# Kernel optimization log

Hardware: AMD Instinct MI355X
Metric: run time of the kernel (lower is better)

## Reference

```python
import jax, jax.numpy as jnp
import numpy as np

N_GROUPS = 32
EPS = 1e-5


def group_norm(x, gamma, beta):
    b, c, h, w = x.shape
    xg = x.reshape(b, N_GROUPS, c // N_GROUPS, h, w)
    mean = xg.mean(axis=(2, 3, 4), keepdims=True)
    var = xg.var(axis=(2, 3, 4), keepdims=True)
    xn = ((xg - mean) * jax.lax.rsqrt(var + EPS)).reshape(b, c, h, w)
    return xn * gamma[None, :, None, None] + beta[None, :, None, None]


def conv1x1(x, W, b):
    # x: [b,c,h,w], W: [out,in], b: [out]
    return jnp.einsum('bchw,oc->bohw', x, W) + b[None, :, None, None]


def setup_inputs() -> dict:
    key = jax.random.key(0)
    ks = jax.random.split(key, 6)
    B, C, H, W = 8, 256, 64, 64
    s = 1.0 / np.sqrt(C)
    return {
        'x': jax.random.normal(ks[0], (B, C, H, W), dtype=jnp.float32),
        'norm_gamma': jnp.ones((C,), jnp.float32),
        'norm_beta': jnp.zeros((C,), jnp.float32),
        'Wq': jax.random.normal(ks[1], (C, C), jnp.float32) * s,
        'bq': jnp.zeros((C,), jnp.float32),
        'Wk': jax.random.normal(ks[2], (C, C), jnp.float32) * s,
        'bk': jnp.zeros((C,), jnp.float32),
        'Wv': jax.random.normal(ks[3], (C, C), jnp.float32) * s,
        'bv': jnp.zeros((C,), jnp.float32),
        'Wo': jax.random.normal(ks[4], (C, C), jnp.float32) * s,
        'bo': jnp.zeros((C,), jnp.float32),
    }


def reference(x, norm_gamma, norm_beta, Wq, bq, Wk, bk, Wv, bv, Wo, bo):
    b, c, h, w = x.shape
    hn = group_norm(x, norm_gamma, norm_beta)
    q = conv1x1(hn, Wq, bq).reshape(b, c, h * w)  # [b,c,hw]
    k = conv1x1(hn, Wk, bk).reshape(b, c, h * w)
    v = conv1x1(hn, Wv, bv).reshape(b, c, h * w)
    # scores[b,i,j] = sum_c q[b,c,i] * k[b,c,j]; scale is int(c)*-0.5
    # (faithful to the source, which multiplies by -0.5*c, NOT c**-0.5)
    scores = jnp.einsum('bci,bcj->bij', q, k) * (c * -0.5)
    attn = jax.nn.softmax(scores, axis=2)  # softmax over j (keys)
    # h_[b,c,i] = sum_j v[b,c,j] * attn[b,i,j]
    h_ = jnp.einsum('bcj,bij->bci', v, attn).reshape(b, c, h, w)
    # source applies self.out to the ORIGINAL input x and adds attention output
    return h_ + conv1x1(x, Wo, bo)
```

## Files before the change

### kernel.cpp

```cpp
#include <hip/hip_runtime.h>
#include <hip/hip_bf16.h>


typedef __attribute__((ext_vector_type(8))) short bf16x8;
typedef __attribute__((ext_vector_type(4))) short s16x4;
typedef __attribute__((ext_vector_type(8))) short s16x8;
typedef __attribute__((ext_vector_type(4))) float f32x4;

#define MFMA16(a, b, c) __builtin_amdgcn_mfma_f32_16x16x32_bf16((a), (b), (c), 0, 0, 0)

#define SCALE_Q (-184.66496523378734f)

__device__ __forceinline__ short f2bf(float f) {
  unsigned int u = __builtin_bit_cast(unsigned int, f);
  u = (u + 0x7FFFu + ((u >> 16) & 1u)) >> 16;
  return (short)(unsigned short)u;
}
__device__ __forceinline__ float bf2f(short h) {
  unsigned int u = ((unsigned int)(unsigned short)h) << 16;
  return __builtin_bit_cast(float, u);
}
__device__ __forceinline__ void async16(void* lds, const void* g) {
  __builtin_amdgcn_global_load_lds(
      (const __attribute__((address_space(1))) unsigned int*)g,
      (__attribute__((address_space(3))) unsigned int*)lds, 16, 0, 0);
}

__global__ void wsplit_k(const float* __restrict__ Wq, const float* __restrict__ Wk,
                         const float* __restrict__ Wv, const float* __restrict__ Wo,
                         short* __restrict__ whi, short* __restrict__ wlo) {
  int idx = blockIdx.x * 256 + threadIdx.x;
  int m = idx >> 16;
  int e = idx & 65535;
  const float* W = (m == 0) ? Wq : (m == 1) ? Wk : (m == 2) ? Wv : Wo;
  float v = W[e];
  short h = f2bf(v);
  whi[idx] = h;
  wlo[idx] = f2bf(v - bf2f(h));
}

__global__ void gn_stats_k(const float* __restrict__ x, float* __restrict__ stats) {
  int bg = blockIdx.x;
  int tid = threadIdx.x;
  const float* p = x + (size_t)bg * 32768;
  float s = 0.f, sq = 0.f;
  for (int it = 0; it < 32; ++it) {
    f32x4 v = *(const f32x4*)(p + (size_t)(it * 256 + tid) * 4);
    s += v[0] + v[1] + v[2] + v[3];
    sq += v[0] * v[0] + v[1] * v[1] + v[2] * v[2] + v[3] * v[3];
  }
#pragma unroll
  for (int off = 1; off < 64; off <<= 1) {
    s += __shfl_xor(s, off);
    sq += __shfl_xor(sq, off);
  }
  __shared__ float ls[4], lq[4];
  int w = tid >> 6;
  if ((tid & 63) == 0) { ls[w] = s; lq[w] = sq; }
  __syncthreads();
  if (tid == 0) {
    float S = ls[0] + ls[1] + ls[2] + ls[3];
    float Q = lq[0] + lq[1] + lq[2] + lq[3];
    float mean = S * (1.f / 32768.f);
    float var = Q * (1.f / 32768.f) - mean * mean;
    stats[bg * 2] = mean;
    stats[bg * 2 + 1] = rsqrtf(var + 1e-5f);
  }
}

__global__ void gn_apply_k(const float* __restrict__ x, const float* __restrict__ gamma,
                           const float* __restrict__ beta, const float* __restrict__ stats,
                           short* __restrict__ hn_hi, short* __restrict__ hn_lo) {
  __shared__ float tile[64 * 68];
  int tid = threadIdx.x;
  int b = blockIdx.z, c0 = blockIdx.y * 64, i0 = blockIdx.x * 64;
  int cc = tid >> 4, ich = tid & 15;
#pragma unroll
  for (int it = 0; it < 4; ++it) {
    int c = c0 + cc + it * 16;
    f32x4 vx = *(const f32x4*)(x + ((size_t)(b * 256 + c)) * 4096 + i0 + ich * 4);
    float mean = stats[(b * 32 + (c >> 3)) * 2];
    float rstd = stats[(b * 32 + (c >> 3)) * 2 + 1];
    float ga = gamma[c] * rstd;
    float be = beta[c] - mean * ga;
    f32x4 h = {vx[0] * ga + be, vx[1] * ga + be, vx[2] * ga + be, vx[3] * ga + be};
    *(f32x4*)(&tile[(cc + it * 16) * 68 + ich * 4]) = h;
  }
  __syncthreads();
  int il = tid >> 2, ch = tid & 3;
  s16x8 hv0, hv1, lv0, lv1;
#pragma unroll
  for (int u = 0; u < 16; ++u) {
    float vv = tile[(ch * 16 + u) * 68 + il];
    short h = f2bf(vv);
    short lo = f2bf(vv - bf2f(h));
    if (u < 8) { hv0[u] = h; lv0[u] = lo; } else { hv1[u - 8] = h; lv1[u - 8] = lo; }
  }
  size_t ro = ((size_t)(b * 4096 + i0 + il)) * 256 + c0 + ch * 16;
  *(s16x8*)(hn_hi + ro) = hv0;
  *(s16x8*)(hn_hi + ro + 8) = hv1;
  *(s16x8*)(hn_lo + ro) = lv0;
  *(s16x8*)(hn_lo + ro + 8) = lv1;
}

__global__ __launch_bounds__(256) void proj_qk_k(
    const short* __restrict__ hn_hi, const short* __restrict__ hn_lo,
    const short* __restrict__ whi, const short* __restrict__ wlo,
    const float* __restrict__ bq, const float* __restrict__ bk,
    short* __restrict__ q_hi, short* __restrict__ q_lo,
    short* __restrict__ k_hi, short* __restrict__ k_lo) {
  int tid = threadIdx.x, w = tid >> 6, lane = tid & 63, l4 = lane & 15, g = lane >> 4;
  int iblk = blockIdx.x, y = blockIdx.y, b = blockIdx.z;
  const short* wh = whi + y * 65536;
  const short* wl = wlo + y * 65536;
  const float* bias = y ? bk : bq;
  short* ohi = (y ? k_hi : q_hi) + (size_t)b * 1048576;
  short* olo = (y ? k_lo : q_lo) + (size_t)b * 1048576;
  float scale = y ? 1.0f : SCALE_Q;
  int arow = iblk * 64 + w * 16 + l4;
  const short* ha = hn_hi + ((size_t)(b * 4096 + arow)) * 256 + g * 8;
  const short* la = hn_lo + ((size_t)(b * 4096 + arow)) * 256 + g * 8;
  f32x4 acc[16];
#pragma unroll
  for (int i = 0; i < 16; ++i) acc[i] = (f32x4){0.f, 0.f, 0.f, 0.f};
  for (int ks = 0; ks < 8; ++ks) {
    bf16x8 ah = *(const bf16x8*)(ha + ks * 32);
    bf16x8 al = *(const bf16x8*)(la + ks * 32);
#pragma unroll
    for (int ct = 0; ct < 16; ++ct) {
      bf16x8 bh = *(const bf16x8*)(wh + (ct * 16 + l4) * 256 + ks * 32 + g * 8);
      bf16x8 bl = *(const bf16x8*)(wl + (ct * 16 + l4) * 256 + ks * 32 + g * 8);
      acc[ct] = MFMA16(ah, bh, acc[ct]);
      acc[ct] = MFMA16(al, bh, acc[ct]);
      acc[ct] = MFMA16(ah, bl, acc[ct]);
    }
  }
  int orow = iblk * 64 + w * 16 + g * 4;
#pragma unroll
  for (int ct = 0; ct < 16; ++ct) {
    int c = ct * 16 + l4;
    float bsv = bias[c];
#pragma unroll
    for (int r = 0; r < 4; ++r) {
      float val = (acc[ct][r] + bsv) * scale;
      short h = f2bf(val);
      short lo = f2bf(val - bf2f(h));
      size_t off = ((size_t)(orow + r)) * 256 + c;
      ohi[off] = h;
      olo[off] = lo;
    }
  }
}

__global__ __launch_bounds__(256) void proj_v_k(
    const short* __restrict__ hn_hi, const short* __restrict__ wv_hi,
    const float* __restrict__ bv, short* __restrict__ vout) {
  int tid = threadIdx.x, w = tid >> 6, lane = tid & 63, l4 = lane & 15, g = lane >> 4;
  int jblk = blockIdx.x, cblk = blockIdx.y, b = blockIdx.z;
  int crow = cblk * 64 + w * 16 + l4;
  const short* ap = wv_hi + (size_t)crow * 256 + g * 8;
  f32x4 acc[4];
#pragma unroll
  for (int i = 0; i < 4; ++i) acc[i] = (f32x4){0.f, 0.f, 0.f, 0.f};
  for (int ks = 0; ks < 8; ++ks) {
    bf16x8 a = *(const bf16x8*)(ap + ks * 32);
#pragma unroll
    for (int jt = 0; jt < 4; ++jt) {
      bf16x8 bb = *(const bf16x8*)(hn_hi +
          ((size_t)(b * 4096 + jblk * 64 + jt * 16 + l4)) * 256 + ks * 32 + g * 8);
      acc[jt] = MFMA16(a, bb, acc[jt]);
    }
  }
#pragma unroll
  for (int jt = 0; jt < 4; ++jt) {
#pragma unroll
    for (int r = 0; r < 4; ++r) {
      int c = cblk * 64 + w * 16 + g * 4 + r;
      int j = jblk * 64 + jt * 16 + l4;
      float val = acc[jt][r] + bv[c];
      vout[((size_t)(b * 256 + c)) * 4096 + j] = f2bf(val);
    }
  }
}

__global__ __launch_bounds__(256, 2) void flash3_k(
    const short* __restrict__ qhi, const short* __restrict__ qlo,
    const short* __restrict__ khi, const short* __restrict__ klo,
    const short* __restrict__ vv, const float* __restrict__ x,
    const short* __restrict__ wo_hi, const float* __restrict__ bo,
    float* __restrict__ out) {
  __shared__ short k_hi_s[2][8192];
  __shared__ short k_lo_s[2][8192];
  __shared__ short p_s[2048];
  __shared__ __attribute__((aligned(16))) float albuf[64];
  __shared__ __attribute__((aligned(16))) float flagbuf[4];
  __shared__ __attribute__((aligned(16))) float lsmbuf[64];

  int tid = threadIdx.x, w = tid >> 6, lane = tid & 63, l4 = lane & 15, g = lane >> 4;
  int b = blockIdx.y, i0 = blockIdx.x * 64;
  size_t boff = (size_t)b * 1048576;
  const short* qh_p = qhi + boff;
  const short* ql_p = qlo + boff;
  const char* kh_g = (const char*)(khi + boff);
  const char* kl_g = (const char*)(klo + boff);
  const short* v_p = vv + boff;

  int qrow = i0 + w * 16 + l4;
  bf16x8 qh[8], ql[8];
#pragma unroll
  for (int ks = 0; ks < 8; ++ks) {
    qh[ks] = *(const bf16x8*)(qh_p + (size_t)qrow * 256 + ks * 32 + g * 8);
    ql[ks] = *(const bf16x8*)(ql_p + (size_t)qrow * 256 + ks * 32 + g * 8);
  }

  f32x4 oac[4][4];
#pragma unroll
  for (int it = 0; it < 4; ++it)
#pragma unroll
    for (int ct = 0; ct < 4; ++ct) oac[it][ct] = (f32x4){0.f, 0.f, 0.f, 0.f};
  float m_cur = -1e30f, lsum = 0.f;

  int sx = (l4 & 7) << 4;
  int colx[8];
#pragma unroll
  for (int ks = 0; ks < 8; ++ks) colx[ks] = (ks * 64 + g * 16) ^ sx;
  int krow_b = l4 * 512;

  int ksrc[4];
#pragma unroll
  for (int it = 0; it < 4; ++it) {
    int d = tid * 16 + it * 4096;
    int krow = d >> 9, kcol = d & 511;
    ksrc[it] = krow * 512 + (kcol ^ ((krow & 7) << 4));
  }

  char* khs = (char*)k_hi_s;
  char* kls = (char*)k_lo_s;
  char* ps = (char*)p_s;
  int cbase = w * 64;
  bf16x8 vreg[4];

#pragma unroll
  for (int it = 0; it < 4; ++it) {
    int ldst = w * 1024 + it * 4096;
    async16(khs + ldst, kh_g + ksrc[it]);
    async16(kls + ldst, kl_g + ksrc[it]);
  }

  for (int js = 0; js < 128; ++js) {
    int cur = (js & 1) * 16384;
    __syncthreads();
    if (js < 127) {
      int kgo = (js + 1) * 16384;
      int nxt = ((js + 1) & 1) * 16384;
#pragma unroll
      for (int it = 0; it < 4; ++it) {
        int ldst = nxt + w * 1024 + it * 4096;
        async16(khs + ldst, kh_g + kgo + ksrc[it]);
        async16(kls + ldst, kl_g + kgo + ksrc[it]);
      }
    }
#pragma unroll
    for (int ct = 0; ct < 4; ++ct)
      vreg[ct] = *(const bf16x8*)(v_p + (size_t)(cbase + ct * 16 + l4) * 4096 +
                                  js * 32 + g * 8);

    f32x4 st0 = (f32x4){0.f, 0.f, 0.f, 0.f};
    f32x4 st1 = (f32x4){0.f, 0.f, 0.f, 0.f};
    __builtin_amdgcn_s_setprio(1);
#pragma unroll
    for (int ks = 0; ks < 8; ++ks) {
      bf16x8 kh0 = *(const bf16x8*)(khs + cur + krow_b + colx[ks]);
      bf16x8 kh1 = *(const bf16x8*)(khs + cur + krow_b + colx[ks] + 8192);
      bf16x8 kl0 = *(const bf16x8*)(kls + cur + krow_b + colx[ks]);
      bf16x8 kl1 = *(const bf16x8*)(kls + cur + krow_b + colx[ks] + 8192);
      st0 = MFMA16(kh0, qh[ks], st0);
      st1 = MFMA16(kh1, qh[ks], st1);
      st0 = MFMA16(kl0, qh[ks], st0);
      st1 = MFMA16(kl1, qh[ks], st1);
      st0 = MFMA16(kh0, ql[ks], st0);
      st1 = MFMA16(kh1, ql[ks], st1);
    }
    __builtin_amdgcn_s_setprio(0);

    float pmax = fmaxf(fmaxf(fmaxf(st0[0], st0[1]), fmaxf(st0[2], st0[3])),
                       fmaxf(fmaxf(st1[0], st1[1]), fmaxf(st1[2], st1[3])));
    pmax = fmaxf(pmax, __shfl_xor(pmax, 16));
    pmax = fmaxf(pmax, __shfl_xor(pmax, 32));
    float alpha = 1.0f;
    bool upd = !__all(pmax <= m_cur + 11.0f);
    if (upd) {
      float m_new = fmaxf(m_cur, pmax);
      alpha = exp2f(m_cur - m_new);
      lsum *= alpha;
      m_cur = m_new;
    }
    f32x4 e0, e1;
#pragma unroll
    for (int r = 0; r < 4; ++r) {
      e0[r] = exp2f(st0[r] - m_cur);
      e1[r] = exp2f(st1[r] - m_cur);
    }
    float lps = e0[0] + e0[1] + e0[2] + e0[3] + e1[0] + e1[1] + e1[2] + e1[3];
    lps += __shfl_xor(lps, 16);
    lps += __shfl_xor(lps, 32);
    lsum += lps;

    s16x4 pw0 = {f2bf(e0[0]), f2bf(e0[1]), f2bf(e0[2]), f2bf(e0[3])};
    s16x4 pw1 = {f2bf(e1[0]), f2bf(e1[1]), f2bf(e1[2]), f2bf(e1[3])};
    int wb = (w * 16 + l4) * 64 + g * 8;
    *(s16x4*)(ps + wb) = pw0;
    *(s16x4*)(ps + wb + 32) = pw1;
    if (lane < 16) albuf[w * 16 + lane] = alpha;
    if (lane == 0) flagbuf[w] = upd ? 1.f : 0.f;

    __syncthreads();

    f32x4 fl = *(const f32x4*)(&flagbuf[0]);
    if (fl[0] + fl[1] + fl[2] + fl[3] > 0.f) {
#pragma unroll
      for (int it = 0; it < 4; ++it) {
        f32x4 av = *(const f32x4*)(&albuf[it * 16 + g * 4]);
#pragma unroll
        for (int ct = 0; ct < 4; ++ct)
#pragma unroll
          for (int r = 0; r < 4; ++r) oac[it][ct][r] *= av[r];
      }
    }
#pragma unroll
    for (int it = 0; it < 4; ++it) {
      bf16x8 pf = *(const bf16x8*)(ps + (it * 16 + l4) * 64 + g * 16);
#pragma unroll
      for (int ct = 0; ct < 4; ++ct) oac[it][ct] = MFMA16(pf, vreg[ct], oac[it][ct]);
    }
  }

  if (lane < 16) lsmbuf[w * 16 + lane] = lsum;
  __syncthreads();
#pragma unroll
  for (int it = 0; it < 4; ++it) {
    f32x4 lv = *(const f32x4*)(&lsmbuf[it * 16 + g * 4]);
    f32x4 iv = {1.f / lv[0], 1.f / lv[1], 1.f / lv[2], 1.f / lv[3]};
#pragma unroll
    for (int ct = 0; ct < 4; ++ct)
#pragma unroll
      for (int r = 0; r < 4; ++r) oac[it][ct][r] *= iv[r];
  }
  const float* xb = x + (size_t)b * 1048576;
  for (int ks = 0; ks < 8; ++ks) {
    bf16x8 af[4], bfr[4];
#pragma unroll
    for (int it = 0; it < 4; ++it) {
#pragma unroll
      for (int e = 0; e < 8; ++e) {
        float xv = xb[(size_t)(ks * 32 + g * 8 + e) * 4096 + i0 + it * 16 + l4];
        af[it][e] = f2bf(xv);
      }
    }
#pragma unroll
    for (int ct = 0; ct < 4; ++ct)
      bfr[ct] = *(const bf16x8*)(wo_hi + (cbase + ct * 16 + l4) * 256 + ks * 32 + g * 8);
#pragma unroll
    for (int it = 0; it < 4; ++it)
#pragma unroll
      for (int ct = 0; ct < 4; ++ct) oac[it][ct] = MFMA16(af[it], bfr[ct], oac[it][ct]);
  }
  float* ob = out + (size_t)b * 1048576;
#pragma unroll
  for (int ct = 0; ct < 4; ++ct) {
    float bov = bo[cbase + ct * 16 + l4];
#pragma unroll
    for (int it = 0; it < 4; ++it) {
      float* ad = ob + (size_t)(cbase + ct * 16 + l4) * 4096 + i0 + it * 16 + g * 4;
      f32x4 res;
#pragma unroll
      for (int r = 0; r < 4; ++r) res[r] = oac[it][ct][r] + bov;
      *(f32x4*)ad = res;
    }
  }
}

extern "C" void kernel_launch(void* const* d_in, const int* in_sizes, int n_in,
                              void* d_out, int out_size, void* d_ws, size_t ws_size,
                              hipStream_t stream) {
  (void)in_sizes; (void)n_in; (void)out_size; (void)ws_size;
  const float* x = (const float*)d_in[0];
  const float* gamma = (const float*)d_in[1];
  const float* beta = (const float*)d_in[2];
  const float* Wq = (const float*)d_in[3];
  const float* bq = (const float*)d_in[4];
  const float* Wk = (const float*)d_in[5];
  const float* bk = (const float*)d_in[6];
  const float* Wv = (const float*)d_in[7];
  const float* bv = (const float*)d_in[8];
  const float* Wo = (const float*)d_in[9];
  const float* bo = (const float*)d_in[10];
  float* out = (float*)d_out;
  char* ws = (char*)d_ws;

  const size_t MB16 = 16777216;
  float* stats = (float*)(ws);
  short* whi = (short*)(ws + 4096);
  short* wlo = (short*)(ws + 4096 + 524288);
  char* base = ws + 4096 + 2 * 524288;
  short* hnhi = (short*)(base);
  short* hnlo = (short*)(base + MB16);
  short* qhi = (short*)(base + 2 * MB16);
  short* qlo = (short*)(base + 3 * MB16);
  short* khi = (short*)(base + 4 * MB16);
  short* klo = (short*)(base + 5 * MB16);
  short* vvp = (short*)(base + 6 * MB16);

  wsplit_k<<<dim3(1024), dim3(256), 0, stream>>>(Wq, Wk, Wv, Wo, whi, wlo);
  gn_stats_k<<<dim3(256), dim3(256), 0, stream>>>(x, stats);
  gn_apply_k<<<dim3(64, 4, 8), dim3(256), 0, stream>>>(x, gamma, beta, stats, hnhi, hnlo);
  proj_qk_k<<<dim3(64, 2, 8), dim3(256), 0, stream>>>(hnhi, hnlo, whi, wlo, bq, bk,
                                                      qhi, qlo, khi, klo);
  proj_v_k<<<dim3(64, 4, 8), dim3(256), 0, stream>>>(hnhi, whi + 2 * 65536, bv, vvp);
  flash3_k<<<dim3(64, 8), dim3(256), 0, stream>>>(qhi, qlo, khi, klo, vvp, x,
                                                  whi + 3 * 65536, bo, out);
}
```

Before: 537.3 us.

## Fuse group-norm kernels and tune flash loop barriers, priority and rounding

Merges the group-norm statistics and apply kernels into one kernel per (batch, group), so the raw input is re-read right after the stats without a separate launch or stats buffer. In the attention kernel, the V register loads move ahead of the async K prefetch, and the mid-loop __syncthreads becomes an explicit lgkmcnt wait plus barrier. MFMA issue priority is raised around the PV product, and bf16 rounding of P and x becomes truncation. The grid is also reordered so batch is the fast block index, which changes L2 locality. Truncation adds a small accuracy bias, and the fused norm does uncoalesced strided column reads into fewer blocks.

```diff
diff --git a/kernel.cpp b/kernel.cpp
--- a/kernel.cpp
+++ b/kernel.cpp
@@ -16,6 +16,9 @@
   u = (u + 0x7FFFu + ((u >> 16) & 1u)) >> 16;
   return (short)(unsigned short)u;
 }
+__device__ __forceinline__ short t2bf(float f) {
+  return (short)(__builtin_bit_cast(unsigned int, f) >> 16);
+}
 __device__ __forceinline__ float bf2f(short h) {
   unsigned int u = ((unsigned int)(unsigned short)h) << 16;
   return __builtin_bit_cast(float, u);
@@ -24,6 +27,11 @@
   __builtin_amdgcn_global_load_lds(
       (const __attribute__((address_space(1))) unsigned int*)g,
       (__attribute__((address_space(3))) unsigned int*)lds, 16, 0, 0);
+}
+__device__ __forceinline__ void lgkm_barrier() {
+  asm volatile("s_waitcnt lgkmcnt(0)" ::: "memory");
+  __builtin_amdgcn_s_barrier();
+  __builtin_amdgcn_sched_barrier(0);
 }
 
 __global__ void wsplit_k(const float* __restrict__ Wq, const float* __restrict__ Wk,
@@ -39,10 +47,12 @@
   wlo[idx] = f2bf(v - bf2f(h));
 }
 
-__global__ void gn_stats_k(const float* __restrict__ x, float* __restrict__ stats) {
-  int bg = blockIdx.x;
-  int tid = threadIdx.x;
-  const float* p = x + (size_t)bg * 32768;
+__global__ __launch_bounds__(256) void gn_fused_k(
+    const float* __restrict__ x, const float* __restrict__ gamma,
+    const float* __restrict__ beta, short* __restrict__ hn_hi,
+    short* __restrict__ hn_lo) {
+  int b = blockIdx.x, g = blockIdx.y, tid = threadIdx.x;
+  const float* p = x + ((size_t)(b * 32 + g)) * 32768;
   float s = 0.f, sq = 0.f;
   for (int it = 0; it < 32; ++it) {
     f32x4 v = *(const f32x4*)(p + (size_t)(it * 256 + tid) * 4);
@@ -55,52 +65,34 @@
     sq += __shfl_xor(sq, off);
   }
   __shared__ float ls[4], lq[4];
-  int w = tid >> 6;
-  if ((tid & 63) == 0) { ls[w] = s; lq[w] = sq; }
+  if ((tid & 63) == 0) { ls[tid >> 6] = s; lq[tid >> 6] = sq; }
   __syncthreads();
-  if (tid == 0) {
-    float S = ls[0] + ls[1] + ls[2] + ls[3];
-    float Q = lq[0] + lq[1] + lq[2] + lq[3];
-    float mean = S * (1.f / 32768.f);
-    float var = Q * (1.f / 32768.f) - mean * mean;
-    stats[bg * 2] = mean;
-    stats[bg * 2 + 1] = rsqrtf(var + 1e-5f);
-  }
-}
-
-__global__ void gn_apply_k(const float* __restrict__ x, const float* __restrict__ gamma,
-                           const float* __restrict__ beta, const float* __restrict__ stats,
-                           short* __restrict__ hn_hi, short* __restrict__ hn_lo) {
-  __shared__ float tile[64 * 68];
-  int tid = threadIdx.x;
-  int b = blockIdx.z, c0 = blockIdx.y * 64, i0 = blockIdx.x * 64;
-  int cc = tid >> 4, ich = tid & 15;
-#pragma unroll
-  for (int it = 0; it < 4; ++it) {
-    int c = c0 + cc + it * 16;
-    f32x4 vx = *(const f32x4*)(x + ((size_t)(b * 256 + c)) * 4096 + i0 + ich * 4);
-    float mean = stats[(b * 32 + (c >> 3)) * 2];
-    float rstd = stats[(b * 32 + (c >> 3)) * 2 + 1];
-    float ga = gamma[c] * rstd;
-    float be = beta[c] - mean * ga;
-    f32x4 h = {vx[0] * ga + be, vx[1] * ga + be, vx[2] * ga + be, vx[3] * ga + be};
-    *(f32x4*)(&tile[(cc + it * 16) * 68 + ich * 4]) = h;
-  }
-  __syncthreads();
-  int il = tid >> 2, ch = tid & 3;
-  s16x8 hv0, hv1, lv0, lv1;
-#pragma unroll
-  for (int u = 0; u < 16; ++u) {
-    float vv = tile[(ch * 16 + u) * 68 + il];
-    short h = f2bf(vv);
-    short lo = f2bf(vv - bf2f(h));
-    if (u < 8) { hv0[u] = h; lv0[u] = lo; } else { hv1[u - 8] = h; lv1[u - 8] = lo; }
-  }
-  size_t ro = ((size_t)(b * 4096 + i0 + il)) * 256 + c0 + ch * 16;
-  *(s16x8*)(hn_hi + ro) = hv0;
-  *(s16x8*)(hn_hi + ro + 8) = hv1;
-  *(s16x8*)(hn_lo + ro) = lv0;
-  *(s16x8*)(hn_lo + ro + 8) = lv1;
+  float S = ls[0] + ls[1] + ls[2] + ls[3];
+  float Q = lq[0] + lq[1] + lq[2] + lq[3];
+  float mean = S * (1.f / 32768.f);
+  float rstd = rsqrtf(Q * (1.f / 32768.f) - mean * mean + 1e-5f);
+  int c0 = g * 8;
+  float ga[8], be[8];
+#pragma unroll
+  for (int cc = 0; cc < 8; ++cc) {
+    ga[cc] = gamma[c0 + cc] * rstd;
+    be[cc] = beta[c0 + cc] - mean * ga[cc];
+  }
+  for (int it = 0; it < 16; ++it) {
+    int i = it * 256 + tid;
+    s16x8 hv, lv;
+#pragma unroll
+    for (int cc = 0; cc < 8; ++cc) {
+      float xv = p[(size_t)cc * 4096 + i];
+      float h = xv * ga[cc] + be[cc];
+      short hh = f2bf(h);
+      hv[cc] = hh;
+      lv[cc] = f2bf(h - bf2f(hh));
+    }
+    size_t ro = ((size_t)(b * 4096 + i)) * 256 + c0;
+    *(s16x8*)(hn_hi + ro) = hv;
+    *(s16x8*)(hn_lo + ro) = lv;
+  }
 }
 
 __global__ __launch_bounds__(256) void proj_qk_k(
@@ -183,7 +175,7 @@
   }
 }
 
-__global__ __launch_bounds__(256, 2) void flash3_k(
+__global__ __launch_bounds__(256, 2) void flash3b_k(
     const short* __restrict__ qhi, const short* __restrict__ qlo,
     const short* __restrict__ khi, const short* __restrict__ klo,
     const short* __restrict__ vv, const float* __restrict__ x,
@@ -197,7 +189,7 @@
   __shared__ __attribute__((aligned(16))) float lsmbuf[64];
 
   int tid = threadIdx.x, w = tid >> 6, lane = tid & 63, l4 = lane & 15, g = lane >> 4;
-  int b = blockIdx.y, i0 = blockIdx.x * 64;
+  int b = blockIdx.x, i0 = blockIdx.y * 64;
   size_t boff = (size_t)b * 1048576;
   const short* qh_p = qhi + boff;
   const short* ql_p = qlo + boff;
@@ -250,6 +242,10 @@
   for (int js = 0; js < 128; ++js) {
     int cur = (js & 1) * 16384;
     __syncthreads();
+#pragma unroll
+    for (int ct = 0; ct < 4; ++ct)
+      vreg[ct] = *(const bf16x8*)(v_p + (size_t)(cbase + ct * 16 + l4) * 4096 +
+                                  js * 32 + g * 8);
     if (js < 127) {
       int kgo = (js + 1) * 16384;
       int nxt = ((js + 1) & 1) * 16384;
@@ -260,10 +256,6 @@
         async16(kls + ldst, kl_g + kgo + ksrc[it]);
       }
     }
-#pragma unroll
-    for (int ct = 0; ct < 4; ++ct)
-      vreg[ct] = *(const bf16x8*)(v_p + (size_t)(cbase + ct * 16 + l4) * 4096 +
-                                  js * 32 + g * 8);
 
     f32x4 st0 = (f32x4){0.f, 0.f, 0.f, 0.f};
     f32x4 st1 = (f32x4){0.f, 0.f, 0.f, 0.f};
@@ -306,15 +298,15 @@
     lps += __shfl_xor(lps, 32);
     lsum += lps;
 
-    s16x4 pw0 = {f2bf(e0[0]), f2bf(e0[1]), f2bf(e0[2]), f2bf(e0[3])};
-    s16x4 pw1 = {f2bf(e1[0]), f2bf(e1[1]), f2bf(e1[2]), f2bf(e1[3])};
+    s16x4 pw0 = {t2bf(e0[0]), t2bf(e0[1]), t2bf(e0[2]), t2bf(e0[3])};
+    s16x4 pw1 = {t2bf(e1[0]), t2bf(e1[1]), t2bf(e1[2]), t2bf(e1[3])};
     int wb = (w * 16 + l4) * 64 + g * 8;
     *(s16x4*)(ps + wb) = pw0;
     *(s16x4*)(ps + wb + 32) = pw1;
     if (lane < 16) albuf[w * 16 + lane] = alpha;
     if (lane == 0) flagbuf[w] = upd ? 1.f : 0.f;
 
-    __syncthreads();
+    lgkm_barrier();
 
     f32x4 fl = *(const f32x4*)(&flagbuf[0]);
     if (fl[0] + fl[1] + fl[2] + fl[3] > 0.f) {
@@ -327,12 +319,14 @@
           for (int r = 0; r < 4; ++r) oac[it][ct][r] *= av[r];
       }
     }
+    __builtin_amdgcn_s_setprio(1);
 #pragma unroll
     for (int it = 0; it < 4; ++it) {
       bf16x8 pf = *(const bf16x8*)(ps + (it * 16 + l4) * 64 + g * 16);
 #pragma unroll
       for (int ct = 0; ct < 4; ++ct) oac[it][ct] = MFMA16(pf, vreg[ct], oac[it][ct]);
     }
+    __builtin_amdgcn_s_setprio(0);
   }
 
   if (lane < 16) lsmbuf[w * 16 + lane] = lsum;
@@ -354,7 +348,7 @@
 #pragma unroll
       for (int e = 0; e < 8; ++e) {
         float xv = xb[(size_t)(ks * 32 + g * 8 + e) * 4096 + i0 + it * 16 + l4];
-        af[it][e] = f2bf(xv);
+        af[it][e] = t2bf(xv);
       }
     }
 #pragma unroll
@@ -399,7 +393,6 @@
   char* ws = (char*)d_ws;
 
   const size_t MB16 = 16777216;
-  float* stats = (float*)(ws);
   short* whi = (short*)(ws + 4096);
   short* wlo = (short*)(ws + 4096 + 524288);
   char* base = ws + 4096 + 2 * 524288;
@@ -412,11 +405,10 @@
   short* vvp = (short*)(base + 6 * MB16);
 
   wsplit_k<<<dim3(1024), dim3(256), 0, stream>>>(Wq, Wk, Wv, Wo, whi, wlo);
-  gn_stats_k<<<dim3(256), dim3(256), 0, stream>>>(x, stats);
-  gn_apply_k<<<dim3(64, 4, 8), dim3(256), 0, stream>>>(x, gamma, beta, stats, hnhi, hnlo);
+  gn_fused_k<<<dim3(8, 32), dim3(256), 0, stream>>>(x, gamma, beta, hnhi, hnlo);
   proj_qk_k<<<dim3(64, 2, 8), dim3(256), 0, stream>>>(hnhi, hnlo, whi, wlo, bq, bk,
                                                       qhi, qlo, khi, klo);
   proj_v_k<<<dim3(64, 4, 8), dim3(256), 0, stream>>>(hnhi, whi + 2 * 65536, bv, vvp);
-  flash3_k<<<dim3(64, 8), dim3(256), 0, stream>>>(qhi, qlo, khi, klo, vvp, x,
-                                                  whi + 3 * 65536, bo, out);
-}
+  flash3b_k<<<dim3(8, 64), dim3(256), 0, stream>>>(qhi, qlo, khi, klo, vvp, x,
+                                                   whi + 3 * 65536, bo, out);
+}
```

Result: no change. 537.9 us (+0.1%).
